# Kernel tuning notes

Measured on AMD Instinct MI355X. Metric: run time of the kernel, lower is better.

## Reference

```python
import jax, jax.numpy as jnp
import numpy as np

DIM = 512
NUM_HEADS = 8
HEAD_DIM = DIM // NUM_HEADS
SEGMENT_LENGTHS = (1024, 2048, 4096)
DILATED_RATIOS = (1, 2, 4)
SCALE = HEAD_DIM ** -0.5
NEG_FILL = -100000000.0  # matches torch masked_fill value


def setup_inputs() -> dict:
    key = jax.random.key(0)
    ks = jax.random.split(key, 8)
    b, L = 2, 8192
    def nrm(k, shape, s=1.0):
        return jax.random.normal(k, shape, dtype=jnp.float32) * s
    return {
        "query": nrm(ks[0], (b, L, DIM)),
        "key_": nrm(ks[1], (b, L, DIM)),
        "value": nrm(ks[2], (b, L, DIM)),
        "Wq": nrm(ks[3], (DIM, DIM), DIM ** -0.5),
        "Wk": nrm(ks[4], (DIM, DIM), DIM ** -0.5),
        "Wv": nrm(ks[5], (DIM, DIM), DIM ** -0.5),
        "Wo": nrm(ks[6], (DIM, DIM), DIM ** -0.5),
        "bo": nrm(ks[7], (DIM,), 0.01),
    }


def _branch(q, k, v, sl, dr):
    """One (segment_length, dilation) branch.
    q,k,v: (b, L, H, D). Returns dense out (b, L, H, D) and lse (b, L, H),
    with uncovered positions set to (0, NEG_FILL).
    gathering/dense_to_sparse reduces, per head hd, to selecting positions
    l*dr + (hd // (H//dr)) within each segment (diagonal of the r1 x r2 block).
    """
    b, L, H, D = q.shape
    n = L // sl          # segments per sequence
    hsub = H // dr       # heads per dilation offset
    lsub = sl // dr      # kept tokens per segment
    # (lsub, H): dilated position of each kept token for each head
    pos = jnp.arange(lsub)[:, None] * dr + (jnp.arange(H) // hsub)[None, :]
    hid = jnp.arange(H)[None, :]

    def gather(x):
        xs = x.reshape(b, n, sl, H, D)
        g = xs[:, :, pos, hid, :]                  # (b, n, lsub, H, D)
        return jnp.transpose(g, (0, 1, 3, 2, 4))    # (b, n, H, lsub, D)

    qi = gather(q) * SCALE
    ki = gather(k)
    vi = gather(v)
    scores = jnp.einsum('bnhld,bnhmd->bnhlm', qi, ki)
    lse = jax.nn.logsumexp(scores, axis=-1)                                  # (b, n, H, lsub)
    p = jax.nn.softmax(scores.astype(jnp.float32), axis=-1).astype(scores.dtype)
    o = jnp.einsum('bnhlm,bnhmd->bnhld', p, vi)                              # (b, n, H, lsub, D)
    # sparse_to_dense: scatter back onto dilated positions (diag_embed)
    o_ = jnp.transpose(o, (0, 1, 3, 2, 4))                                    # (b, n, lsub, H, D)
    od = jnp.zeros((b, n, sl, H, D), o.dtype).at[:, :, pos, hid, :].set(o_)
    ld = jnp.zeros((b, n, sl, H), lse.dtype).at[:, :, pos, hid].set(
        jnp.transpose(lse, (0, 1, 3, 2)))
    ld = jnp.where(ld == 0, NEG_FILL, ld)  # masked_fill_(lse == 0, -1e8)
    return od.reshape(b, L, H, D), ld.reshape(b, L, H)


def reference(query, key_, value, Wq, Wk, Wv, Wo, bo):
    b, L, _ = query.shape
    def heads(x, W):
        return (x @ W.T).reshape(b, L, NUM_HEADS, HEAD_DIM)
    q = heads(query, Wq)
    k = heads(key_, Wk)
    v = heads(value, Wv)
    outs, lses = [], []
    for sl, dr in zip(SEGMENT_LENGTHS, DILATED_RATIOS):
        o, l = _branch(q, k, v, sl, dr)
        outs.append(o)
        lses.append(l)
    # merge branches via logsumexp-weighted combination (weights detached in torch)
    lse_stack = jnp.stack(lses, 0)            # (nb, b, L, H)
    m = lse_stack.max(0)
    w = jnp.exp(lse_stack - m)
    w = w / w.sum(0)
    w = jax.lax.stop_gradient(w)
    out = sum(o * wi[..., None] for o, wi in zip(outs, list(w)))
    out = out.reshape(b, L, DIM)
    return out @ Wo.T + bo
```

## Files before the change

### kernel.cpp

```cpp
#include <hip/hip_runtime.h>
#include <hip/hip_bf16.h>

typedef unsigned short u16;
typedef unsigned int u32;
typedef __attribute__((ext_vector_type(8))) short short8;
typedef __attribute__((ext_vector_type(4))) float floatx4;
typedef __attribute__((ext_vector_type(2))) unsigned int uint2v;

__device__ __forceinline__ float b2f(u16 u) {
    u32 x = ((u32)u) << 16;
    return __builtin_bit_cast(float, x);
}
__device__ __forceinline__ u16 f2b(float f) {
    u32 x = __builtin_bit_cast(u32, f);
    return (u16)((x + 0x7fffu + ((x >> 16) & 1u)) >> 16);
}
__device__ __forceinline__ u32 pack2(float lo, float hi) {
    float2 f; f.x = lo; f.y = hi;
    __hip_bfloat162 h = __float22bfloat162_rn(f);
    u32 r;
    __builtin_memcpy(&r, &h, 4);
    return r;
}
__device__ __forceinline__ float fexp2(float x) {
#if __has_builtin(__builtin_amdgcn_exp2f)
    return __builtin_amdgcn_exp2f(x);
#else
    return __expf(x * 0.6931471805599453f);
#endif
}

__device__ __forceinline__ uint2v pl32(u32 a, u32 b) {
    return __builtin_amdgcn_permlane32_swap(a, b, false, false);
}

__device__ __forceinline__ void gl16(const u16* g, u16* l) {
    __builtin_amdgcn_global_load_lds(
        (const __attribute__((address_space(1))) void*)g,
        (__attribute__((address_space(3))) void*)l, 16, 0, 0);
}

template<bool AF32>
__global__ __launch_bounds__(256) void gemm_bt_bias(
    const void* __restrict__ Ap, const float* __restrict__ B,
    u16* __restrict__ Cb, float* __restrict__ Cf, const float* __restrict__ bias,
    int M, int N, int K, float scale)
{
    __shared__ __align__(16) u16 a_lds[128][72];
    __shared__ __align__(16) u16 b_lds[128][72];
    const int tid = threadIdx.x;
    const int lane = tid & 63, wv = tid >> 6;
    const int quad = lane >> 4, l15 = lane & 15;
    const int tm = blockIdx.x, tn = blockIdx.y;
    const int wm = (wv >> 1) * 64, wn = (wv & 1) * 64;
    (void)M;

    floatx4 acc[4][4];
#pragma unroll
    for (int i = 0; i < 4; ++i)
#pragma unroll
        for (int j = 0; j < 4; ++j) acc[i][j] = (floatx4)0.f;

    for (int k0 = 0; k0 < K; k0 += 64) {
#pragma unroll
        for (int r = 0; r < 4; ++r) {
            int idx = r * 256 + tid;
            int row = idx >> 3, ch = (idx & 7) * 8;
            if constexpr (AF32) {
                const float* A = (const float*)Ap;
                const float* src = A + (size_t)(tm * 128 + row) * K + k0 + ch;
                float4 f0 = *(const float4*)src;
                float4 f1 = *(const float4*)(src + 4);
                uint4 pk;
                pk.x = pack2(f0.x, f0.y);
                pk.y = pack2(f0.z, f0.w);
                pk.z = pack2(f1.x, f1.y);
                pk.w = pack2(f1.z, f1.w);
                *(uint4*)&a_lds[row][ch] = pk;
            } else {
                const u16* A = (const u16*)Ap;
                *(uint4*)&a_lds[row][ch] =
                    *(const uint4*)(A + (size_t)(tm * 128 + row) * K + k0 + ch);
            }
            {
                const float* src = B + (size_t)(tn * 128 + row) * K + k0 + ch;
                float4 f0 = *(const float4*)src;
                float4 f1 = *(const float4*)(src + 4);
                uint4 pk;
                pk.x = pack2(f0.x, f0.y);
                pk.y = pack2(f0.z, f0.w);
                pk.z = pack2(f1.x, f1.y);
                pk.w = pack2(f1.z, f1.w);
                *(uint4*)&b_lds[row][ch] = pk;
            }
        }
        __syncthreads();
#pragma unroll
        for (int dc = 0; dc < 2; ++dc) {
            short8 af[4], bf[4];
#pragma unroll
            for (int mi = 0; mi < 4; ++mi)
                af[mi] = *(const short8*)&a_lds[wm + mi * 16 + l15][dc * 32 + quad * 8];
#pragma unroll
            for (int ni = 0; ni < 4; ++ni)
                bf[ni] = *(const short8*)&b_lds[wn + ni * 16 + l15][dc * 32 + quad * 8];
#pragma unroll
            for (int mi = 0; mi < 4; ++mi)
#pragma unroll
                for (int ni = 0; ni < 4; ++ni)
                    acc[mi][ni] = __builtin_amdgcn_mfma_f32_16x16x32_bf16(
                        af[mi], bf[ni], acc[mi][ni], 0, 0, 0);
        }
        __syncthreads();
    }
#pragma unroll
    for (int mi = 0; mi < 4; ++mi)
#pragma unroll
        for (int ni = 0; ni < 4; ++ni) {
            int col = tn * 128 + wn + ni * 16 + l15;
            float bb = bias ? bias[col] : 0.f;
#pragma unroll
            for (int r = 0; r < 4; ++r) {
                int row = tm * 128 + wm + mi * 16 + quad * 4 + r;
                float val = acc[mi][ni][r] * scale + bb;
                if (Cf) Cf[(size_t)row * N + col] = val;
                else    Cb[(size_t)row * N + col] = f2b(val);
            }
        }
}

__device__ __forceinline__ void decode_inst(int inst, int& b, int& s, int& h,
                                            int& sl, int& dr, int& phase)
{
    if (inst < 128)      { int j = inst;       b = j >> 6; s = (j >> 3) & 7; h = j & 7; sl = 1024; dr = 1; phase = 0;      }
    else if (inst < 192) { int j = inst - 128; b = j >> 5; s = (j >> 3) & 3; h = j & 7; sl = 2048; dr = 2; phase = h >> 2; }
    else                 { int j = inst - 192; b = j >> 4; s = (j >> 3) & 1; h = j & 7; sl = 4096; dr = 4; phase = h >> 1; }
}

__global__ __launch_bounds__(256) void gather_kv(
    const u16* __restrict__ kk, const u16* __restrict__ vv,
    u16* __restrict__ KG, u16* __restrict__ VT)
{
    int inst = blockIdx.x;
    int b, s, h, sl, dr, phase;
    decode_inst(inst, b, s, h, sl, dr, phase);
    int n0 = blockIdx.y * 32;
    __shared__ __align__(16) u16 tile[32][72];
    int tid = threadIdx.x;
    int row = tid >> 3, ch = (tid & 7) * 8;
    int n = n0 + row;
    size_t pos = (size_t)s * sl + (size_t)n * dr + phase;
    size_t src = (((size_t)b * 8192 + pos) * 8 + h) * 64 + ch;
    int chs = ch ^ ((n & 7) * 8);
    *(uint4*)(KG + ((size_t)inst * 1024 + n) * 64 + chs) = *(const uint4*)(kk + src);
    *(uint4*)&tile[row][ch] = *(const uint4*)(vv + src);
    __syncthreads();
    int d = tid >> 2, nn = (tid & 3) * 8;
    __align__(16) u16 tmp[8];
#pragma unroll
    for (int j = 0; j < 8; ++j) tmp[j] = tile[nn + j][d];
    int col = (n0 + nn) ^ ((d & 7) * 8);
    *(uint4*)(VT + ((size_t)inst * 64 + d) * 1024 + col) = *(uint4*)tmp;
}

__global__ __launch_bounds__(256, 4) void attn_kernel(
    const u16* __restrict__ q, const u16* __restrict__ KG,
    const u16* __restrict__ VT, u16* __restrict__ Og, float* __restrict__ Lg)
{
    const int inst = blockIdx.y, qt = blockIdx.x;
    int b, s, h, sl, dr, phase;
    decode_inst(inst, b, s, h, sl, dr, phase);
    __shared__ __align__(16) u16 k_lds[128][64];
    __shared__ __align__(16) u16 vt_lds[64][128];
    const int tid = threadIdx.x, lane = tid & 63, wv = tid >> 6;
    const int quad = lane >> 4, l15 = lane & 15;
    const int sl15 = (l15 & 3) | ((l15 & 4) << 1) | ((l15 & 8) >> 1);
    const int ksw = (sl15 & 7) * 8;
    const int vsw = (l15 & 7) * 8;

    const int qrow = qt * 64 + wv * 16 + l15;
    const size_t qpos = (size_t)s * sl + (size_t)qrow * dr + phase;
    const u16* qbase = q + (((size_t)b * 8192 + qpos) * 8 + h) * 64;
    const short8 qf0 = *(const short8*)(qbase + quad * 8);
    const short8 qf1 = *(const short8*)(qbase + 32 + quad * 8);

    uint4 onesw;
    onesw.x = 0x3F803F80u; onesw.y = 0x3F803F80u;
    onesw.z = 0x3F803F80u; onesw.w = 0x3F803F80u;
    const short8 vones = __builtin_bit_cast(short8, onesw);

    floatx4 oacc[4];
#pragma unroll
    for (int dt = 0; dt < 4; ++dt) oacc[dt] = (floatx4)0.f;
    floatx4 racc = (floatx4)0.f;
    float mst = -1e30f;

    const u16* KGb = KG + (size_t)inst * 65536;
    const u16* VTb = VT + (size_t)inst * 65536;
    u16* klb = &k_lds[0][0];
    u16* vlb = &vt_lds[0][0];

    for (int it = 0; it < 8; ++it) {
        const int k0 = it * 128;
#pragma unroll
        for (int r = 0; r < 4; ++r) {
            int c = wv * 4 + r;
            gl16(KGb + (size_t)k0 * 64 + c * 512 + lane * 8, klb + c * 512);
            gl16(VTb + (size_t)(c * 4 + (lane >> 4)) * 1024 + k0 + (lane & 15) * 8,
                 vlb + c * 512);
        }
        __syncthreads();

        floatx4 sacc[8];
#pragma unroll
        for (int nt = 0; nt < 8; ++nt) {
            sacc[nt] = (floatx4)0.f;
            short8 kf0 = *(const short8*)&k_lds[nt * 16 + sl15][(quad * 8) ^ ksw];
            short8 kf1 = *(const short8*)&k_lds[nt * 16 + sl15][(32 + quad * 8) ^ ksw];
            sacc[nt] = __builtin_amdgcn_mfma_f32_16x16x32_bf16(kf0, qf0, sacc[nt], 0, 0, 0);
            sacc[nt] = __builtin_amdgcn_mfma_f32_16x16x32_bf16(kf1, qf1, sacc[nt], 0, 0, 0);
        }

        float t0, t1;
        {
            float m0 = fmaxf(fmaxf(sacc[0][0], sacc[0][1]), fmaxf(sacc[0][2], sacc[0][3]));
            float m1 = fmaxf(fmaxf(sacc[1][0], sacc[1][1]), fmaxf(sacc[1][2], sacc[1][3]));
            float m2 = fmaxf(fmaxf(sacc[2][0], sacc[2][1]), fmaxf(sacc[2][2], sacc[2][3]));
            float m3 = fmaxf(fmaxf(sacc[3][0], sacc[3][1]), fmaxf(sacc[3][2], sacc[3][3]));
            t0 = fmaxf(fmaxf(m0, m1), fmaxf(m2, m3));
            float m4 = fmaxf(fmaxf(sacc[4][0], sacc[4][1]), fmaxf(sacc[4][2], sacc[4][3]));
            float m5 = fmaxf(fmaxf(sacc[5][0], sacc[5][1]), fmaxf(sacc[5][2], sacc[5][3]));
            float m6 = fmaxf(fmaxf(sacc[6][0], sacc[6][1]), fmaxf(sacc[6][2], sacc[6][3]));
            float m7 = fmaxf(fmaxf(sacc[7][0], sacc[7][1]), fmaxf(sacc[7][2], sacc[7][3]));
            t1 = fmaxf(fmaxf(m4, m5), fmaxf(m6, m7));
        }
        float mx = fmaxf(t0, t1);
        mx = fmaxf(mx, __shfl_xor(mx, 16, 64));
        mx = fmaxf(mx, __shfl_xor(mx, 32, 64));

        if (!__all(mx - mst <= 8.f)) {
            float mnew = fmaxf(mst, mx);
            float alpha = fexp2(mst - mnew);
#pragma unroll
            for (int dt = 0; dt < 4; ++dt) oacc[dt] *= alpha;
            racc *= alpha;
            mst = mnew;
        }

#pragma unroll
        for (int nt = 0; nt < 8; ++nt)
#pragma unroll
            for (int r = 0; r < 4; ++r)
                sacc[nt][r] = fexp2(sacc[nt][r] - mst);

#pragma unroll
        for (int nc = 0; nc < 4; ++nc) {
            u32 pk00 = pack2(sacc[2 * nc][0], sacc[2 * nc][1]);
            u32 pk01 = pack2(sacc[2 * nc][2], sacc[2 * nc][3]);
            u32 pk10 = pack2(sacc[2 * nc + 1][0], sacc[2 * nc + 1][1]);
            u32 pk11 = pack2(sacc[2 * nc + 1][2], sacc[2 * nc + 1][3]);
            uint2v xz = pl32(pk00, pk10);
            uint2v yw = pl32(pk01, pk11);
            uint4 bw;
            bw.x = xz[0];
            bw.y = yw[0];
            bw.z = xz[1];
            bw.w = yw[1];
            short8 pf = __builtin_bit_cast(short8, bw);
#pragma unroll
            for (int dt = 0; dt < 4; ++dt) {
                short8 vf = *(const short8*)
                    &vt_lds[dt * 16 + l15][(nc * 32 + quad * 8) ^ vsw];
                oacc[dt] = __builtin_amdgcn_mfma_f32_16x16x32_bf16(vf, pf, oacc[dt], 0, 0, 0);
            }
            racc = __builtin_amdgcn_mfma_f32_16x16x32_bf16(vones, pf, racc, 0, 0, 0);
        }
        __syncthreads();
    }

    const int esw = (l15 & 7) * 8;
    float lst = racc[0];
    float inv_l = (lst > 0.f) ? (1.f / lst) : 0.f;
#pragma unroll
    for (int dt = 0; dt < 4; ++dt) {
        u32 lo = pack2(oacc[dt][0] * inv_l, oacc[dt][1] * inv_l);
        u32 hi = pack2(oacc[dt][2] * inv_l, oacc[dt][3] * inv_l);
        uint2 v; v.x = lo; v.y = hi;
        *(uint2*)&k_lds[wv * 16 + l15][(dt * 16 + quad * 4) ^ esw] = v;
    }
    __syncthreads();
#pragma unroll
    for (int c = 0; c < 2; ++c) {
        uint4 val = *(const uint4*)&k_lds[wv * 16 + l15][(quad * 16 + c * 8) ^ esw];
        *(uint4*)(Og + (((size_t)inst * 1024 + qt * 64 + wv * 16 + l15) * 64
                        + quad * 16 + c * 8)) = val;
    }
    if (quad == 0) {
        Lg[(size_t)inst * 1024 + qt * 64 + wv * 16 + l15] = mst + __log2f(lst);
    }
}

__global__ __launch_bounds__(256) void merge_kernel(
    const u16* __restrict__ Og, const float* __restrict__ Lg,
    u16* __restrict__ merged)
{
    int bid = blockIdx.x;
    int b = bid >> 13, l = bid & 8191;
    int t = threadIdx.x;
    int h = t >> 5, d0 = (t & 31) * 2;

    int inst0 = b * 64 + ((l >> 10) << 3) + h;
    int row0 = l & 1023;
    int p1 = l & 2047;
    bool c1 = ((p1 & 1) == (h >> 2));
    int inst1 = 128 + b * 32 + ((l >> 11) << 3) + h;
    int row1 = p1 >> 1;
    int p2 = l & 4095;
    bool c2 = ((p2 & 3) == (h >> 1));
    int inst2 = 192 + b * 16 + ((l >> 12) << 3) + h;
    int row2 = p2 >> 2;

    float lse0 = Lg[(size_t)inst0 * 1024 + row0];
    float lse1 = c1 ? Lg[(size_t)inst1 * 1024 + row1] : -1e30f;
    float lse2 = c2 ? Lg[(size_t)inst2 * 1024 + row2] : -1e30f;
    float m = fmaxf(lse0, fmaxf(lse1, lse2));
    float w0 = fexp2(lse0 - m);
    float w1 = c1 ? fexp2(lse1 - m) : 0.f;
    float w2 = c2 ? fexp2(lse2 - m) : 0.f;
    float inv = 1.f / (w0 + w1 + w2);
    w0 *= inv; w1 *= inv; w2 *= inv;

    u32 u0 = *(const u32*)(Og + ((size_t)inst0 * 1024 + row0) * 64 + d0);
    u32 u1 = c1 ? *(const u32*)(Og + ((size_t)inst1 * 1024 + row1) * 64 + d0) : 0u;
    u32 u2 = c2 ? *(const u32*)(Og + ((size_t)inst2 * 1024 + row2) * 64 + d0) : 0u;
    float a0 = b2f((u16)(u0 & 0xffff)), e0 = b2f((u16)(u0 >> 16));
    float a1 = b2f((u16)(u1 & 0xffff)), e1 = b2f((u16)(u1 >> 16));
    float a2 = b2f((u16)(u2 & 0xffff)), e2 = b2f((u16)(u2 >> 16));
    float ra = w0 * a0 + w1 * a1 + w2 * a2;
    float rb = w0 * e0 + w1 * e1 + w2 * e2;
    u32 outp = pack2(ra, rb);
    *(u32*)(merged + (((size_t)b * 8192 + l) * 8 + h) * 64 + d0) = outp;
}

extern "C" void kernel_launch(void* const* d_in, const int* in_sizes, int n_in,
                              void* d_out, int out_size, void* d_ws, size_t ws_size,
                              hipStream_t stream)
{
    (void)in_sizes; (void)n_in; (void)out_size; (void)ws_size;
    const float* query = (const float*)d_in[0];
    const float* key_  = (const float*)d_in[1];
    const float* value = (const float*)d_in[2];
    const float* Wq    = (const float*)d_in[3];
    const float* Wk    = (const float*)d_in[4];
    const float* Wv    = (const float*)d_in[5];
    const float* Wo    = (const float*)d_in[6];
    const float* bo    = (const float*)d_in[7];

    char* ws = (char*)d_ws;
    const size_t SZ_PROJ = (size_t)16384 * 512 * 2;
    const size_t SZ_KG   = (size_t)224 * 1024 * 64 * 2;
    const size_t SZ_LG   = (size_t)224 * 1024 * 4;
    u16*   qb     = (u16*)(ws);
    u16*   kb     = (u16*)(ws + SZ_PROJ);
    u16*   vb     = (u16*)(ws + 2 * SZ_PROJ);
    u16*   KG     = (u16*)(ws + 3 * SZ_PROJ);
    u16*   VT     = (u16*)(ws + 3 * SZ_PROJ + SZ_KG);
    u16*   Og     = (u16*)(ws + 3 * SZ_PROJ + 2 * SZ_KG);
    float* Lg     = (float*)(ws + 3 * SZ_PROJ + 3 * SZ_KG);
    u16*   merged = (u16*)(ws + 3 * SZ_PROJ + 3 * SZ_KG + SZ_LG);

    const int M = 16384, N = 512, K = 512;
    const float SCALE = 0.125f * 1.44269504088896f;

    gemm_bt_bias<true><<<dim3(128, 4), 256, 0, stream>>>(query, Wq, qb, nullptr, nullptr, M, N, K, SCALE);
    gemm_bt_bias<true><<<dim3(128, 4), 256, 0, stream>>>(key_,  Wk, kb, nullptr, nullptr, M, N, K, 1.0f);
    gemm_bt_bias<true><<<dim3(128, 4), 256, 0, stream>>>(value, Wv, vb, nullptr, nullptr, M, N, K, 1.0f);
    gather_kv<<<dim3(224, 32), 256, 0, stream>>>(kb, vb, KG, VT);
    attn_kernel<<<dim3(16, 224), 256, 0, stream>>>(qb, KG, VT, Og, Lg);
    merge_kernel<<<16384, 256, 0, stream>>>(Og, Lg, merged);
    gemm_bt_bias<false><<<dim3(128, 4), 256, 0, stream>>>(merged, Wo, nullptr, (float*)d_out, bo, M, N, K, 1.0f);
}
```

Measured before the change: 341.5 us.

## Pre-convert weights to swizzled bf16 and load GEMM tiles via direct-to-LDS loads

Adds a kernel that converts all four fp32 weight matrices to bf16 once, stored with an XOR swizzle, so the GEMMs stop re-reading and re-converting fp32 weights in every block. B tiles, and the A tile of the output projection (whose merged input is now written pre-swizzled by the merge kernel), are loaded with global_load_lds straight into unpadded swizzled LDS. This cuts weight traffic and conversion ALU work and avoids LDS bank conflicts without padding. It adds an extra launch and a cross-kernel swizzle convention that must stay consistent.

```diff
diff --git a/kernel.cpp b/kernel.cpp
--- a/kernel.cpp
+++ b/kernel.cpp
@@ -40,20 +40,44 @@
         (__attribute__((address_space(3))) void*)l, 16, 0, 0);
 }
 
-template<bool AF32>
+__global__ __launch_bounds__(256) void conv_w(
+    const float* __restrict__ w0, const float* __restrict__ w1,
+    const float* __restrict__ w2, const float* __restrict__ w3,
+    u16* __restrict__ WB)
+{
+    int wsel = blockIdx.x;
+    const float* src = wsel == 0 ? w0 : wsel == 1 ? w1 : wsel == 2 ? w2 : w3;
+    int row = blockIdx.y * 4 + (threadIdx.x >> 6);
+    int ch = (threadIdx.x & 63) * 8;
+    const float* s = src + (size_t)row * 512 + ch;
+    float4 f0 = *(const float4*)s;
+    float4 f1 = *(const float4*)(s + 4);
+    uint4 pk;
+    pk.x = pack2(f0.x, f0.y);
+    pk.y = pack2(f0.z, f0.w);
+    pk.z = pack2(f1.x, f1.y);
+    pk.w = pack2(f1.z, f1.w);
+    int dst = ch ^ ((row & 7) * 8);
+    *(uint4*)(WB + (size_t)wsel * 262144 + (size_t)row * 512 + dst) = pk;
+}
+
+template<int MODE>
 __global__ __launch_bounds__(256) void gemm_bt_bias(
-    const void* __restrict__ Ap, const float* __restrict__ B,
+    const void* __restrict__ Ap, const u16* __restrict__ Bw,
     u16* __restrict__ Cb, float* __restrict__ Cf, const float* __restrict__ bias,
-    int M, int N, int K, float scale)
-{
-    __shared__ __align__(16) u16 a_lds[128][72];
-    __shared__ __align__(16) u16 b_lds[128][72];
+    int N, int K, float scale)
+{
+    constexpr int APAD = (MODE == 0) ? 72 : 64;
+    __shared__ __align__(16) u16 a_lds[128][APAD];
+    __shared__ __align__(16) u16 b_lds[128][64];
     const int tid = threadIdx.x;
     const int lane = tid & 63, wv = tid >> 6;
     const int quad = lane >> 4, l15 = lane & 15;
     const int tm = blockIdx.x, tn = blockIdx.y;
     const int wm = (wv >> 1) * 64, wn = (wv & 1) * 64;
-    (void)M;
+    const int bsw = (l15 & 7) * 8;
+    u16* alb = &a_lds[0][0];
+    u16* blb = &b_lds[0][0];
 
     floatx4 acc[4][4];
 #pragma unroll
@@ -64,9 +88,24 @@
     for (int k0 = 0; k0 < K; k0 += 64) {
 #pragma unroll
         for (int r = 0; r < 4; ++r) {
-            int idx = r * 256 + tid;
-            int row = idx >> 3, ch = (idx & 7) * 8;
-            if constexpr (AF32) {
+            int c = wv * 4 + r;
+            gl16(Bw + (size_t)(tn * 128 + c * 8 + (lane >> 3)) * 512
+                     + k0 + (lane & 7) * 8,
+                 blb + c * 512);
+        }
+        if constexpr (MODE == 1) {
+#pragma unroll
+            for (int r = 0; r < 4; ++r) {
+                int c = wv * 4 + r;
+                gl16((const u16*)Ap + (size_t)(tm * 128 + c * 8 + (lane >> 3)) * 512
+                         + k0 + (lane & 7) * 8,
+                     alb + c * 512);
+            }
+        } else {
+#pragma unroll
+            for (int r = 0; r < 4; ++r) {
+                int idx = r * 256 + tid;
+                int row = idx >> 3, ch = (idx & 7) * 8;
                 const float* A = (const float*)Ap;
                 const float* src = A + (size_t)(tm * 128 + row) * K + k0 + ch;
                 float4 f0 = *(const float4*)src;
@@ -77,21 +116,6 @@
                 pk.z = pack2(f1.x, f1.y);
                 pk.w = pack2(f1.z, f1.w);
                 *(uint4*)&a_lds[row][ch] = pk;
-            } else {
-                const u16* A = (const u16*)Ap;
-                *(uint4*)&a_lds[row][ch] =
-                    *(const uint4*)(A + (size_t)(tm * 128 + row) * K + k0 + ch);
-            }
-            {
-                const float* src = B + (size_t)(tn * 128 + row) * K + k0 + ch;
-                float4 f0 = *(const float4*)src;
-                float4 f1 = *(const float4*)(src + 4);
-                uint4 pk;
-                pk.x = pack2(f0.x, f0.y);
-                pk.y = pack2(f0.z, f0.w);
-                pk.z = pack2(f1.x, f1.y);
-                pk.w = pack2(f1.z, f1.w);
-                *(uint4*)&b_lds[row][ch] = pk;
             }
         }
         __syncthreads();
@@ -99,11 +123,14 @@
         for (int dc = 0; dc < 2; ++dc) {
             short8 af[4], bf[4];
 #pragma unroll
-            for (int mi = 0; mi < 4; ++mi)
-                af[mi] = *(const short8*)&a_lds[wm + mi * 16 + l15][dc * 32 + quad * 8];
+            for (int mi = 0; mi < 4; ++mi) {
+                int col = dc * 32 + quad * 8;
+                if constexpr (MODE == 1) col ^= bsw;
+                af[mi] = *(const short8*)&a_lds[wm + mi * 16 + l15][col];
+            }
 #pragma unroll
             for (int ni = 0; ni < 4; ++ni)
-                bf[ni] = *(const short8*)&b_lds[wn + ni * 16 + l15][dc * 32 + quad * 8];
+                bf[ni] = *(const short8*)&b_lds[wn + ni * 16 + l15][(dc * 32 + quad * 8) ^ bsw];
 #pragma unroll
             for (int mi = 0; mi < 4; ++mi)
 #pragma unroll
@@ -339,7 +366,8 @@
     float ra = w0 * a0 + w1 * a1 + w2 * a2;
     float rb = w0 * e0 + w1 * e1 + w2 * e2;
     u32 outp = pack2(ra, rb);
-    *(u32*)(merged + (((size_t)b * 8192 + l) * 8 + h) * 64 + d0) = outp;
+    int d0s = d0 ^ ((l & 7) * 8);
+    *(u32*)(merged + (((size_t)b * 8192 + l) * 8 + h) * 64 + d0s) = outp;
 }
 
 extern "C" void kernel_launch(void* const* d_in, const int* in_sizes, int n_in,
@@ -368,15 +396,17 @@
     u16*   Og     = (u16*)(ws + 3 * SZ_PROJ + 2 * SZ_KG);
     float* Lg     = (float*)(ws + 3 * SZ_PROJ + 3 * SZ_KG);
     u16*   merged = (u16*)(ws + 3 * SZ_PROJ + 3 * SZ_KG + SZ_LG);
-
-    const int M = 16384, N = 512, K = 512;
+    u16*   WB     = (u16*)(ws + 3 * SZ_PROJ + 3 * SZ_KG + SZ_LG + SZ_PROJ);
+
+    const int N = 512, K = 512;
     const float SCALE = 0.125f * 1.44269504088896f;
 
-    gemm_bt_bias<true><<<dim3(128, 4), 256, 0, stream>>>(query, Wq, qb, nullptr, nullptr, M, N, K, SCALE);
-    gemm_bt_bias<true><<<dim3(128, 4), 256, 0, stream>>>(key_,  Wk, kb, nullptr, nullptr, M, N, K, 1.0f);
-    gemm_bt_bias<true><<<dim3(128, 4), 256, 0, stream>>>(value, Wv, vb, nullptr, nullptr, M, N, K, 1.0f);
+    conv_w<<<dim3(4, 128), 256, 0, stream>>>(Wq, Wk, Wv, Wo, WB);
+    gemm_bt_bias<0><<<dim3(128, 4), 256, 0, stream>>>(query, WB,              qb, nullptr, nullptr, N, K, SCALE);
+    gemm_bt_bias<0><<<dim3(128, 4), 256, 0, stream>>>(key_,  WB + 262144,     kb, nullptr, nullptr, N, K, 1.0f);
+    gemm_bt_bias<0><<<dim3(128, 4), 256, 0, stream>>>(value, WB + 2 * 262144, vb, nullptr, nullptr, N, K, 1.0f);
     gather_kv<<<dim3(224, 32), 256, 0, stream>>>(kb, vb, KG, VT);
     attn_kernel<<<dim3(16, 224), 256, 0, stream>>>(qb, KG, VT, Og, Lg);
     merge_kernel<<<16384, 256, 0, stream>>>(Og, Lg, merged);
-    gemm_bt_bias<false><<<dim3(128, 4), 256, 0, stream>>>(merged, Wo, nullptr, (float*)d_out, bo, M, N, K, 1.0f);
-}
+    gemm_bt_bias<1><<<dim3(128, 4), 256, 0, stream>>>(merged, WB + 3 * 262144, nullptr, (float*)d_out, bo, N, K, 1.0f);
+}
```

After: 325.0 us. 4.8% less time.
